# Kernel optimization log

Hardware: AMD Instinct MI355X
Metric: run time of the kernel (lower is better)

The kernel has to match this reference:

```python
import jax, jax.numpy as jnp
import numpy as np

HID = 64
EPS_LN = 1e-5

def _mlp(x, W, b, g, beta):
    # Linear -> LayerNorm -> ReLU (VectorNet-style MLP)
    h = x @ W + b
    mu = jnp.mean(h, axis=-1, keepdims=True)
    var = jnp.var(h, axis=-1, keepdims=True)
    h = (h - mu) * jax.lax.rsqrt(var + EPS_LN) * g + beta
    return jax.nn.relu(h)

def setup_inputs() -> dict:
    key = jax.random.key(0)
    ks = jax.random.split(key, 8)
    N = 2_000_000
    C_IN = 8
    NSEG = 100_000
    inp = {
        'x': jax.random.normal(ks[0], (N, C_IN), dtype=jnp.float32),
        'category': jax.random.randint(ks[1], (N,), 0, NSEG, dtype=jnp.int64),
        'num_segments': NSEG,
    }
    dims_in = [C_IN, 2 * HID, 2 * HID]
    for i, din in enumerate(dims_in):
        kw = jax.random.fold_in(ks[2], i)
        inp[f'W{i}'] = jax.random.normal(kw, (din, HID), dtype=jnp.float32) / np.sqrt(din)
        inp[f'b{i}'] = jnp.zeros((HID,), dtype=jnp.float32)
        inp[f'g{i}'] = jnp.ones((HID,), dtype=jnp.float32)
        inp[f'be{i}'] = jnp.zeros((HID,), dtype=jnp.float32)
    return inp

def reference(x, category, num_segments, W0, b0, g0, be0, W1, b1, g1, be1, W2, b2, g2, be2):
    cat = category.astype(jnp.int32)
    params = [(W0, b0, g0, be0), (W1, b1, g1, be1), (W2, b2, g2, be2)]
    for W, b, g, beta in params:
        h = _mlp(x, W, b, g, beta)                              # [N, HID]
        agg = jax.ops.segment_max(h, cat, num_segments=num_segments)  # [NSEG, HID]
        x = jnp.concatenate([h, agg[cat]], axis=-1)             # [N, 2*HID]
    # column-wise L2 normalization over the node dimension
    col_norm = jnp.linalg.norm(x, axis=0)                       # [2*HID]
    return x / (col_norm + 1e-12)
```

## Files before the change

kernel.cpp:

```cpp
#include <hip/hip_runtime.h>

#define HID 64

__global__ __launch_bounds__(256) void k_hist(const int* __restrict__ cat, int n,
                                              unsigned* __restrict__ counts) {
  int i = blockIdx.x * blockDim.x + threadIdx.x;
  if (i < n) atomicAdd(&counts[cat[i]], 1u);
}

__global__ __launch_bounds__(1024) void k_scan1(const unsigned* __restrict__ counts, int nseg,
                                                unsigned* __restrict__ lexcl,
                                                unsigned* __restrict__ btot) {
  __shared__ unsigned s[1024];
  int t = threadIdx.x;
  int base = blockIdx.x * 1024;
  unsigned v = (base + t < nseg) ? counts[base + t] : 0u;
  s[t] = v;
  __syncthreads();
  for (int o = 1; o < 1024; o <<= 1) {
    unsigned add = (t >= o) ? s[t - o] : 0u;
    __syncthreads();
    s[t] += add;
    __syncthreads();
  }
  if (base + t < nseg) lexcl[base + t] = s[t] - v;
  if (t == 1023) btot[blockIdx.x] = s[1023];
}

__global__ void k_scan2(unsigned* __restrict__ btot, int nb) {
  if (blockIdx.x == 0 && threadIdx.x == 0) {
    unsigned run = 0;
    for (int i = 0; i < nb; i++) { unsigned v = btot[i]; btot[i] = run; run += v; }
  }
}

__global__ __launch_bounds__(256) void k_scan3(const unsigned* __restrict__ lexcl,
                                               const unsigned* __restrict__ btot,
                                               int nseg, int n,
                                               unsigned* __restrict__ offsets,
                                               unsigned* __restrict__ cursor) {
  int i = blockIdx.x * blockDim.x + threadIdx.x;
  if (i < nseg) {
    unsigned o = lexcl[i] + btot[i >> 10];
    offsets[i] = o;
    cursor[i] = o;
  }
  if (i == 0) offsets[nseg] = (unsigned)n;
}

__global__ __launch_bounds__(256) void k_fill(const int* __restrict__ cat, int n,
                                              unsigned* __restrict__ cursor,
                                              unsigned* __restrict__ rowidx) {
  int i = blockIdx.x * blockDim.x + threadIdx.x;
  if (i < n) {
    unsigned p = atomicAdd(&cursor[cat[i]], 1u);
    rowidx[p] = (unsigned)i;
  }
}

template <int CIN, bool HAS_AP>
__global__ __launch_bounds__(256) void k_mlp(const float* __restrict__ xin, int xstride,
                                             const float* __restrict__ W,
                                             const float* __restrict__ bias,
                                             const float* __restrict__ ap,
                                             const int* __restrict__ cat,
                                             const float* __restrict__ g,
                                             const float* __restrict__ be,
                                             float* __restrict__ hout, int ostride, int n) {
  int r = blockIdx.x * blockDim.x + threadIdx.x;
  if (r >= n) return;
  const float* xr = xin + (long)r * xstride;

  float4 a[16];
  if (HAS_AP) {
    const float4* apr = (const float4*)(ap + (long)cat[r] * HID);
#pragma unroll
    for (int j = 0; j < 16; j++) a[j] = apr[j];
  } else {
    const float4* b4 = (const float4*)bias;
#pragma unroll
    for (int j = 0; j < 16; j++) a[j] = b4[j];
  }

#pragma unroll 4
  for (int k4 = 0; k4 < CIN / 4; k4++) {
    float4 xv = ((const float4*)xr)[k4];
    float xs[4] = {xv.x, xv.y, xv.z, xv.w};
#pragma unroll
    for (int kk = 0; kk < 4; kk++) {
      float xk = xs[kk];
      const float4* w4 = (const float4*)(W + (k4 * 4 + kk) * HID);
#pragma unroll
      for (int j = 0; j < 16; j++) {
        float4 w = w4[j];
        a[j].x = fmaf(xk, w.x, a[j].x);
        a[j].y = fmaf(xk, w.y, a[j].y);
        a[j].z = fmaf(xk, w.z, a[j].z);
        a[j].w = fmaf(xk, w.w, a[j].w);
      }
    }
  }

  float s1 = 0.f, s2 = 0.f;
#pragma unroll
  for (int j = 0; j < 16; j++) {
    s1 += a[j].x + a[j].y + a[j].z + a[j].w;
    s2 += a[j].x * a[j].x + a[j].y * a[j].y + a[j].z * a[j].z + a[j].w * a[j].w;
  }
  float mu = s1 * (1.f / 64.f);
  float var = s2 * (1.f / 64.f) - mu * mu;
  float rs = rsqrtf(var + 1e-5f);

  const float4* g4 = (const float4*)g;
  const float4* be4 = (const float4*)be;
  float* orow = hout + (long)r * ostride;
#pragma unroll
  for (int j = 0; j < 16; j++) {
    float4 gg = g4[j], bb = be4[j];
    float4 o;
    o.x = fmaxf(fmaf((a[j].x - mu) * rs, gg.x, bb.x), 0.f);
    o.y = fmaxf(fmaf((a[j].y - mu) * rs, gg.y, bb.y), 0.f);
    o.z = fmaxf(fmaf((a[j].z - mu) * rs, gg.z, bb.z), 0.f);
    o.w = fmaxf(fmaf((a[j].w - mu) * rs, gg.w, bb.w), 0.f);
    ((float4*)orow)[j] = o;
  }
}

template <bool PROJ>
__global__ __launch_bounds__(256) void k_agg(const float* __restrict__ h, int hstride,
                                             const unsigned* __restrict__ offsets,
                                             const unsigned* __restrict__ rowidx,
                                             const float* __restrict__ Wbot,
                                             const float* __restrict__ bias,
                                             float* __restrict__ outbuf, int nseg) {
  int wid = (int)(((long)blockIdx.x * blockDim.x + threadIdx.x) >> 6);
  int lane = threadIdx.x & 63;
  if (wid >= nseg) return;
  unsigned i0 = offsets[wid], i1 = offsets[wid + 1];
  float m = 0.f;
#pragma unroll 4
  for (unsigned i = i0; i < i1; i++) {
    unsigned rr = rowidx[i];
    m = fmaxf(m, h[(long)rr * hstride + lane]);
  }
  if (!PROJ) {
    outbuf[(long)wid * HID + lane] = m;
    return;
  }
  float acc = bias[lane];
#pragma unroll 8
  for (int k = 0; k < HID; k++) {
    float ak = __shfl(m, k, 64);
    acc = fmaf(ak, Wbot[k * HID + lane], acc);
  }
  outbuf[(long)wid * HID + lane] = acc;
}

__global__ __launch_bounds__(256) void k_colsq(const float* __restrict__ h2, int stride, int n,
                                               float* __restrict__ part ) {
  int c = threadIdx.x & 63;
  int rg = threadIdx.x >> 6;
  float acc = 0.f;
  for (long r = (long)blockIdx.x * 4 + rg; r < n; r += (long)gridDim.x * 4) {
    float v = h2[r * stride + c];
    acc += v * v;
  }
  __shared__ float sm[256];
  sm[threadIdx.x] = acc;
  __syncthreads();
  if (threadIdx.x < 64) {
    float t = sm[threadIdx.x] + sm[threadIdx.x + 64] + sm[threadIdx.x + 128] + sm[threadIdx.x + 192];
    atomicAdd(&part[(blockIdx.x & 255) * 128 + threadIdx.x], t);
  }
}

__global__ __launch_bounds__(256) void k_normtail(const float* __restrict__ agg2,
                                                  const unsigned* __restrict__ counts, int nseg,
                                                  float* __restrict__ part) {
  int c = threadIdx.x & 63;
  int sg = threadIdx.x >> 6;
  float acc = 0.f;
  for (int s = blockIdx.x * 4 + sg; s < nseg; s += gridDim.x * 4) {
    float v = agg2[(long)s * HID + c];
    acc += (float)counts[s] * v * v;
  }
  __shared__ float sm[256];
  sm[threadIdx.x] = acc;
  __syncthreads();
  if (threadIdx.x < 64) {
    float t = sm[threadIdx.x] + sm[threadIdx.x + 64] + sm[threadIdx.x + 128] + sm[threadIdx.x + 192];
    atomicAdd(&part[(blockIdx.x & 255) * 128 + 64 + threadIdx.x], t);
  }
}

__global__ void k_normfinal(const float* __restrict__ part, float* __restrict__ invn) {
  int j = threadIdx.x;
  if (j < 128) {
    float s = 0.f;
    for (int i = 0; i < 256; i++) s += part[i * 128 + j];
    invn[j] = 1.f / (sqrtf(s) + 1e-12f);
  }
}

__global__ __launch_bounds__(256) void k_final(float* __restrict__ out,
                                               const float* __restrict__ agg2,
                                               const int* __restrict__ cat,
                                               const float* __restrict__ invn, int n) {
  long i4 = (long)blockIdx.x * blockDim.x + threadIdx.x;
  long r = i4 >> 5;
  int c4 = (int)(i4 & 31);
  if (r >= n) return;
  int c = c4 * 4;
  float4 inv = *(const float4*)(invn + c);
  float4 v;
  if (c < 64) {
    v = *(const float4*)(out + r * 128 + c);
  } else {
    v = *(const float4*)(agg2 + (long)cat[r] * HID + (c - 64));
  }
  v.x *= inv.x; v.y *= inv.y; v.z *= inv.z; v.w *= inv.w;
  *(float4*)(out + r * 128 + c) = v;
}

extern "C" void kernel_launch(void* const* d_in, const int* in_sizes, int n_in,
                              void* d_out, int out_size, void* d_ws, size_t ws_size,
                              hipStream_t stream) {
  const float* x = (const float*)d_in[0];
  const int* cat = (const int*)d_in[1];
  const float* W0 = (const float*)d_in[3];
  const float* b0 = (const float*)d_in[4];
  const float* g0 = (const float*)d_in[5];
  const float* be0 = (const float*)d_in[6];
  const float* W1 = (const float*)d_in[7];
  const float* b1 = (const float*)d_in[8];
  const float* g1 = (const float*)d_in[9];
  const float* be1 = (const float*)d_in[10];
  const float* W2 = (const float*)d_in[11];
  const float* b2 = (const float*)d_in[12];
  const float* g2 = (const float*)d_in[13];
  const float* be2 = (const float*)d_in[14];

  const int N = in_sizes[1];
  const int NSEG = 100000;
  float* out = (float*)d_out;

  char* ws = (char*)d_ws;
  size_t off = 0;
  auto alloc = [&](size_t bytes) -> void* {
    void* p = (void*)(ws + off);
    off = (off + bytes + 511) & ~(size_t)511;
    return p;
  };
  float* h1 = (float*)alloc((size_t)N * HID * 4);
  float* apj = (float*)alloc((size_t)NSEG * HID * 4);
  float* agg2 = (float*)alloc((size_t)NSEG * HID * 4);
  unsigned* rowidx = (unsigned*)alloc((size_t)N * 4);
  unsigned* counts = (unsigned*)alloc((size_t)NSEG * 4);
  unsigned* offsets = (unsigned*)alloc((size_t)(NSEG + 1) * 4);
  unsigned* lexcl = (unsigned*)alloc((size_t)NSEG * 4);
  unsigned* cursor = (unsigned*)alloc((size_t)NSEG * 4);
  unsigned* btot = (unsigned*)alloc(4096);
  float* part = (float*)alloc(256 * 128 * 4);
  float* invn = (float*)alloc(128 * 4);

  hipMemsetAsync(counts, 0, (size_t)NSEG * 4, stream);
  hipMemsetAsync(part, 0, 256 * 128 * 4, stream);

  const int TB = 256;
  const int gridN = (N + TB - 1) / TB;

  k_hist<<<gridN, TB, 0, stream>>>(cat, N, counts);
  int nb = (NSEG + 1023) / 1024;
  k_scan1<<<nb, 1024, 0, stream>>>(counts, NSEG, lexcl, btot);
  k_scan2<<<1, 64, 0, stream>>>(btot, nb);
  k_scan3<<<(NSEG + TB - 1) / TB, TB, 0, stream>>>(lexcl, btot, NSEG, N, offsets, cursor);
  k_fill<<<gridN, TB, 0, stream>>>(cat, N, cursor, rowidx);

  float* h0 = out + 64;
  float* h2 = out;
  const int gseg = NSEG / 4;

  k_mlp<8, false><<<gridN, TB, 0, stream>>>(x, 8, W0, b0, nullptr, nullptr, g0, be0, h0, 128, N);
  k_agg<true><<<gseg, TB, 0, stream>>>(h0, 128, offsets, rowidx, W1 + 64 * HID, b1, apj, NSEG);
  k_mlp<64, true><<<gridN, TB, 0, stream>>>(h0, 128, W1, nullptr, apj, cat, g1, be1, h1, HID, N);
  k_agg<true><<<gseg, TB, 0, stream>>>(h1, HID, offsets, rowidx, W2 + 64 * HID, b2, apj, NSEG);
  k_mlp<64, true><<<gridN, TB, 0, stream>>>(h1, HID, W2, nullptr, apj, cat, g2, be2, h2, 128, N);
  k_agg<false><<<gseg, TB, 0, stream>>>(h2, 128, offsets, rowidx, nullptr, nullptr, agg2, NSEG);

  k_colsq<<<2048, TB, 0, stream>>>(h2, 128, N, part);
  k_normtail<<<512, TB, 0, stream>>>(agg2, counts, NSEG, part);
  k_normfinal<<<1, 128, 0, stream>>>(part, invn);

  k_final<<<(int)(((long)N * 32 + TB - 1) / TB), TB, 0, stream>>>(out, agg2, cat, invn, N);
}
```

Measured before the change: 3.740 ms.

## Recompute layer-0 MLP inside layer-1 kernel, packed FMA, fuse colsq into agg

Layer-1 MLP now recomputes layer-0 Linear+LN+ReLU from x in registers instead of reading h0 back, so h0 is only written once for aggregation. GEMMs use 2-wide float vectors so the compiler can emit packed FMA. All hidden states live in one compact 64-wide buffer reused in place, and the column-square sum moves into the last segment-max pass, which removes the separate colsq kernel. The final kernel assembles the strided output from the compact buffer. The cost is extra recomputation and higher register pressure in the fused kernel.

```diff
diff --git a/kernel.cpp b/kernel.cpp
--- a/kernel.cpp
+++ b/kernel.cpp
@@ -1,6 +1,7 @@
 #include <hip/hip_runtime.h>
 
 #define HID 64
+typedef __attribute__((ext_vector_type(2))) float f32x2;
 
 __global__ __launch_bounds__(256) void k_hist(const int* __restrict__ cat, int n,
                                               unsigned* __restrict__ counts) {
@@ -58,119 +59,168 @@
   }
 }
 
-template <int CIN, bool HAS_AP>
-__global__ __launch_bounds__(256) void k_mlp(const float* __restrict__ xin, int xstride,
-                                             const float* __restrict__ W,
-                                             const float* __restrict__ bias,
-                                             const float* __restrict__ ap,
-                                             const int* __restrict__ cat,
-                                             const float* __restrict__ g,
-                                             const float* __restrict__ be,
-                                             float* __restrict__ hout, int ostride, int n) {
-  int r = blockIdx.x * blockDim.x + threadIdx.x;
+__device__ __forceinline__ void init_acc_from4(f32x2 acc[32], const float4* __restrict__ src) {
+#pragma unroll
+  for (int j = 0; j < 16; ++j) {
+    float4 t = src[j];
+    acc[2 * j][0] = t.x; acc[2 * j][1] = t.y;
+    acc[2 * j + 1][0] = t.z; acc[2 * j + 1][1] = t.w;
+  }
+}
+
+template <int NK4>
+__device__ __forceinline__ void gemm_stream(const float4* __restrict__ x4,
+                                            const float* __restrict__ W,
+                                            f32x2 acc[32]) {
+#pragma unroll 4
+  for (int k4 = 0; k4 < NK4; ++k4) {
+    float4 xv = x4[k4];
+    const float* Wb = W + k4 * 4 * HID;
+    float xs[4] = {xv.x, xv.y, xv.z, xv.w};
+#pragma unroll
+    for (int kk = 0; kk < 4; ++kk) {
+      f32x2 xb; xb[0] = xs[kk]; xb[1] = xs[kk];
+      const f32x2* wr = (const f32x2*)(Wb + kk * HID);
+#pragma unroll
+      for (int j = 0; j < 32; ++j) acc[j] += xb * wr[j];
+    }
+  }
+}
+
+__device__ __forceinline__ void gemm_reg(const f32x2 xr[32],
+                                         const float* __restrict__ W,
+                                         f32x2 acc[32]) {
+#pragma unroll
+  for (int k = 0; k < 64; ++k) {
+    float xk = xr[k >> 1][k & 1];
+    f32x2 xb; xb[0] = xk; xb[1] = xk;
+    const f32x2* wr = (const f32x2*)(W + k * HID);
+#pragma unroll
+    for (int j = 0; j < 32; ++j) acc[j] += xb * wr[j];
+  }
+}
+
+__device__ __forceinline__ void ln_relu(const f32x2 acc[32], const float* __restrict__ g,
+                                        const float* __restrict__ be, f32x2 o[32]) {
+  f32x2 s1; s1[0] = 0.f; s1[1] = 0.f;
+  f32x2 s2; s2[0] = 0.f; s2[1] = 0.f;
+#pragma unroll
+  for (int j = 0; j < 32; ++j) { s1 += acc[j]; s2 += acc[j] * acc[j]; }
+  float mu = (s1[0] + s1[1]) * (1.f / 64.f);
+  float var = (s2[0] + s2[1]) * (1.f / 64.f) - mu * mu;
+  float rs = rsqrtf(var + 1e-5f);
+  const f32x2* g2 = (const f32x2*)g;
+  const f32x2* be2 = (const f32x2*)be;
+#pragma unroll
+  for (int j = 0; j < 32; ++j) {
+    f32x2 t = (acc[j] - mu) * rs * g2[j] + be2[j];
+    f32x2 z; z[0] = fmaxf(t[0], 0.f); z[1] = fmaxf(t[1], 0.f);
+    o[j] = z;
+  }
+}
+
+__device__ __forceinline__ void store_row(float* __restrict__ dst, const f32x2 o[32]) {
+#pragma unroll
+  for (int j = 0; j < 16; ++j) {
+    float4 t;
+    t.x = o[2 * j][0]; t.y = o[2 * j][1];
+    t.z = o[2 * j + 1][0]; t.w = o[2 * j + 1][1];
+    ((float4*)dst)[j] = t;
+  }
+}
+
+__global__ __launch_bounds__(256, 4) void k_mlp0(const float* __restrict__ x,
+    const float* __restrict__ W0, const float* __restrict__ b0,
+    const float* __restrict__ g0, const float* __restrict__ be0,
+    float* __restrict__ h0, int n) {
+  int r = blockIdx.x * 256 + threadIdx.x;
   if (r >= n) return;
-  const float* xr = xin + (long)r * xstride;
-
-  float4 a[16];
-  if (HAS_AP) {
-    const float4* apr = (const float4*)(ap + (long)cat[r] * HID);
-#pragma unroll
-    for (int j = 0; j < 16; j++) a[j] = apr[j];
-  } else {
-    const float4* b4 = (const float4*)bias;
-#pragma unroll
-    for (int j = 0; j < 16; j++) a[j] = b4[j];
-  }
-
-#pragma unroll 4
-  for (int k4 = 0; k4 < CIN / 4; k4++) {
-    float4 xv = ((const float4*)xr)[k4];
-    float xs[4] = {xv.x, xv.y, xv.z, xv.w};
-#pragma unroll
-    for (int kk = 0; kk < 4; kk++) {
-      float xk = xs[kk];
-      const float4* w4 = (const float4*)(W + (k4 * 4 + kk) * HID);
-#pragma unroll
-      for (int j = 0; j < 16; j++) {
-        float4 w = w4[j];
-        a[j].x = fmaf(xk, w.x, a[j].x);
-        a[j].y = fmaf(xk, w.y, a[j].y);
-        a[j].z = fmaf(xk, w.z, a[j].z);
-        a[j].w = fmaf(xk, w.w, a[j].w);
-      }
-    }
-  }
-
-  float s1 = 0.f, s2 = 0.f;
-#pragma unroll
-  for (int j = 0; j < 16; j++) {
-    s1 += a[j].x + a[j].y + a[j].z + a[j].w;
-    s2 += a[j].x * a[j].x + a[j].y * a[j].y + a[j].z * a[j].z + a[j].w * a[j].w;
-  }
-  float mu = s1 * (1.f / 64.f);
-  float var = s2 * (1.f / 64.f) - mu * mu;
-  float rs = rsqrtf(var + 1e-5f);
-
-  const float4* g4 = (const float4*)g;
-  const float4* be4 = (const float4*)be;
-  float* orow = hout + (long)r * ostride;
-#pragma unroll
-  for (int j = 0; j < 16; j++) {
-    float4 gg = g4[j], bb = be4[j];
-    float4 o;
-    o.x = fmaxf(fmaf((a[j].x - mu) * rs, gg.x, bb.x), 0.f);
-    o.y = fmaxf(fmaf((a[j].y - mu) * rs, gg.y, bb.y), 0.f);
-    o.z = fmaxf(fmaf((a[j].z - mu) * rs, gg.z, bb.z), 0.f);
-    o.w = fmaxf(fmaf((a[j].w - mu) * rs, gg.w, bb.w), 0.f);
-    ((float4*)orow)[j] = o;
-  }
-}
-
-template <bool PROJ>
-__global__ __launch_bounds__(256) void k_agg(const float* __restrict__ h, int hstride,
+  f32x2 acc[32];
+  init_acc_from4(acc, (const float4*)b0);
+  gemm_stream<2>((const float4*)(x + (long)r * 8), W0, acc);
+  f32x2 o[32];
+  ln_relu(acc, g0, be0, o);
+  store_row(h0 + (long)r * HID, o);
+}
+
+__global__ __launch_bounds__(256, 3) void k_mlp01(const float* __restrict__ x,
+    const float* __restrict__ W0, const float* __restrict__ b0,
+    const float* __restrict__ g0, const float* __restrict__ be0,
+    const float* __restrict__ W1, const float* __restrict__ apj,
+    const int* __restrict__ cat,
+    const float* __restrict__ g1, const float* __restrict__ be1,
+    float* __restrict__ h1, int n) {
+  int r = blockIdx.x * 256 + threadIdx.x;
+  if (r >= n) return;
+  int c = cat[r];
+  f32x2 acc[32];
+  init_acc_from4(acc, (const float4*)b0);
+  gemm_stream<2>((const float4*)(x + (long)r * 8), W0, acc);
+  f32x2 h0v[32];
+  ln_relu(acc, g0, be0, h0v);
+  init_acc_from4(acc, (const float4*)(apj + (long)c * HID));
+  gemm_reg(h0v, W1, acc);
+  f32x2 o[32];
+  ln_relu(acc, g1, be1, o);
+  store_row(h1 + (long)r * HID, o);
+}
+
+__global__ __launch_bounds__(256, 4) void k_mlp2(float* __restrict__ h,
+    const float* __restrict__ W2, const float* __restrict__ apj,
+    const int* __restrict__ cat,
+    const float* __restrict__ g2, const float* __restrict__ be2, int n) {
+  int r = blockIdx.x * 256 + threadIdx.x;
+  if (r >= n) return;
+  int c = cat[r];
+  f32x2 acc[32];
+  init_acc_from4(acc, (const float4*)(apj + (long)c * HID));
+  gemm_stream<16>((const float4*)(h + (long)r * HID), W2, acc);
+  f32x2 o[32];
+  ln_relu(acc, g2, be2, o);
+  store_row(h + (long)r * HID, o);
+}
+
+template <bool PROJ, bool SQ>
+__global__ __launch_bounds__(256) void k_agg(const float* __restrict__ h,
                                              const unsigned* __restrict__ offsets,
                                              const unsigned* __restrict__ rowidx,
-                                             const float* __restrict__ Wbot,
+                                             const float* __restrict__ Wb,
                                              const float* __restrict__ bias,
-                                             float* __restrict__ outbuf, int nseg) {
-  int wid = (int)(((long)blockIdx.x * blockDim.x + threadIdx.x) >> 6);
+                                             float* __restrict__ outbuf,
+                                             float* __restrict__ part, int nseg) {
+  int wv = threadIdx.x >> 6;
   int lane = threadIdx.x & 63;
-  if (wid >= nseg) return;
-  unsigned i0 = offsets[wid], i1 = offsets[wid + 1];
-  float m = 0.f;
+  int wid = blockIdx.x * 4 + wv;
+  float m = 0.f, sq = 0.f;
+  if (wid < nseg) {
+    unsigned i0 = offsets[wid], i1 = offsets[wid + 1];
 #pragma unroll 4
-  for (unsigned i = i0; i < i1; i++) {
-    unsigned rr = rowidx[i];
-    m = fmaxf(m, h[(long)rr * hstride + lane]);
-  }
-  if (!PROJ) {
-    outbuf[(long)wid * HID + lane] = m;
-    return;
-  }
-  float acc = bias[lane];
+    for (unsigned i = i0; i < i1; ++i) {
+      unsigned rr = rowidx[i];
+      float v = h[(long)rr * HID + lane];
+      m = fmaxf(m, v);
+      if (SQ) sq += v * v;
+    }
+    if (PROJ) {
+      float a = bias[lane];
 #pragma unroll 8
-  for (int k = 0; k < HID; k++) {
-    float ak = __shfl(m, k, 64);
-    acc = fmaf(ak, Wbot[k * HID + lane], acc);
-  }
-  outbuf[(long)wid * HID + lane] = acc;
-}
-
-__global__ __launch_bounds__(256) void k_colsq(const float* __restrict__ h2, int stride, int n,
-                                               float* __restrict__ part ) {
-  int c = threadIdx.x & 63;
-  int rg = threadIdx.x >> 6;
-  float acc = 0.f;
-  for (long r = (long)blockIdx.x * 4 + rg; r < n; r += (long)gridDim.x * 4) {
-    float v = h2[r * stride + c];
-    acc += v * v;
-  }
-  __shared__ float sm[256];
-  sm[threadIdx.x] = acc;
-  __syncthreads();
-  if (threadIdx.x < 64) {
-    float t = sm[threadIdx.x] + sm[threadIdx.x + 64] + sm[threadIdx.x + 128] + sm[threadIdx.x + 192];
-    atomicAdd(&part[(blockIdx.x & 255) * 128 + threadIdx.x], t);
+      for (int k = 0; k < HID; ++k) {
+        float ak = __shfl(m, k, 64);
+        a = fmaf(ak, Wb[k * HID + lane], a);
+      }
+      outbuf[(long)wid * HID + lane] = a;
+    } else {
+      outbuf[(long)wid * HID + lane] = m;
+    }
+  }
+  if (SQ) {
+    __shared__ float sm[256];
+    sm[threadIdx.x] = sq;
+    __syncthreads();
+    if (threadIdx.x < 64) {
+      float t = sm[threadIdx.x] + sm[threadIdx.x + 64] + sm[threadIdx.x + 128] + sm[threadIdx.x + 192];
+      atomicAdd(&part[(blockIdx.x & 255) * 128 + threadIdx.x], t);
+    }
   }
 }
 
@@ -203,23 +253,23 @@
 }
 
 __global__ __launch_bounds__(256) void k_final(float* __restrict__ out,
+                                               const float* __restrict__ h2,
                                                const float* __restrict__ agg2,
                                                const int* __restrict__ cat,
-                                               const float* __restrict__ invn, int n) {
-  long i4 = (long)blockIdx.x * blockDim.x + threadIdx.x;
-  long r = i4 >> 5;
-  int c4 = (int)(i4 & 31);
+                                               const float* __restrict__ invn, long n) {
+  long i8 = (long)blockIdx.x * 256 + threadIdx.x;
+  long r = i8 >> 4;
   if (r >= n) return;
-  int c = c4 * 4;
-  float4 inv = *(const float4*)(invn + c);
-  float4 v;
-  if (c < 64) {
-    v = *(const float4*)(out + r * 128 + c);
-  } else {
-    v = *(const float4*)(agg2 + (long)cat[r] * HID + (c - 64));
-  }
-  v.x *= inv.x; v.y *= inv.y; v.z *= inv.z; v.w *= inv.w;
-  *(float4*)(out + r * 128 + c) = v;
+  int c8 = (int)(i8 & 15) * 8;
+  const float4* src = (c8 < 64) ? (const float4*)(h2 + r * 64 + c8)
+                                : (const float4*)(agg2 + (long)cat[r] * 64 + (c8 - 64));
+  float4 v0 = src[0], v1 = src[1];
+  float4 i0 = *(const float4*)(invn + c8);
+  float4 i1 = *(const float4*)(invn + c8 + 4);
+  v0.x *= i0.x; v0.y *= i0.y; v0.z *= i0.z; v0.w *= i0.w;
+  v1.x *= i1.x; v1.y *= i1.y; v1.z *= i1.z; v1.w *= i1.w;
+  float4* dst = (float4*)(out + r * 128 + c8);
+  dst[0] = v0; dst[1] = v1;
 }
 
 extern "C" void kernel_launch(void* const* d_in, const int* in_sizes, int n_in,
@@ -251,7 +301,7 @@
     off = (off + bytes + 511) & ~(size_t)511;
     return p;
   };
-  float* h1 = (float*)alloc((size_t)N * HID * 4);
+  float* hbuf = (float*)alloc((size_t)N * HID * 4);
   float* apj = (float*)alloc((size_t)NSEG * HID * 4);
   float* agg2 = (float*)alloc((size_t)NSEG * HID * 4);
   unsigned* rowidx = (unsigned*)alloc((size_t)N * 4);
@@ -268,6 +318,7 @@
 
   const int TB = 256;
   const int gridN = (N + TB - 1) / TB;
+  const int gseg = (NSEG + 3) / 4;
 
   k_hist<<<gridN, TB, 0, stream>>>(cat, N, counts);
   int nb = (NSEG + 1023) / 1024;
@@ -276,20 +327,15 @@
   k_scan3<<<(NSEG + TB - 1) / TB, TB, 0, stream>>>(lexcl, btot, NSEG, N, offsets, cursor);
   k_fill<<<gridN, TB, 0, stream>>>(cat, N, cursor, rowidx);
 
-  float* h0 = out + 64;
-  float* h2 = out;
-  const int gseg = NSEG / 4;
-
-  k_mlp<8, false><<<gridN, TB, 0, stream>>>(x, 8, W0, b0, nullptr, nullptr, g0, be0, h0, 128, N);
-  k_agg<true><<<gseg, TB, 0, stream>>>(h0, 128, offsets, rowidx, W1 + 64 * HID, b1, apj, NSEG);
-  k_mlp<64, true><<<gridN, TB, 0, stream>>>(h0, 128, W1, nullptr, apj, cat, g1, be1, h1, HID, N);
-  k_agg<true><<<gseg, TB, 0, stream>>>(h1, HID, offsets, rowidx, W2 + 64 * HID, b2, apj, NSEG);
-  k_mlp<64, true><<<gridN, TB, 0, stream>>>(h1, HID, W2, nullptr, apj, cat, g2, be2, h2, 128, N);
-  k_agg<false><<<gseg, TB, 0, stream>>>(h2, 128, offsets, rowidx, nullptr, nullptr, agg2, NSEG);
-
-  k_colsq<<<2048, TB, 0, stream>>>(h2, 128, N, part);
+  k_mlp0<<<gridN, TB, 0, stream>>>(x, W0, b0, g0, be0, hbuf, N);
+  k_agg<true, false><<<gseg, TB, 0, stream>>>(hbuf, offsets, rowidx, W1 + 64 * HID, b1, apj, nullptr, NSEG);
+  k_mlp01<<<gridN, TB, 0, stream>>>(x, W0, b0, g0, be0, W1, apj, cat, g1, be1, hbuf, N);
+  k_agg<true, false><<<gseg, TB, 0, stream>>>(hbuf, offsets, rowidx, W2 + 64 * HID, b2, apj, nullptr, NSEG);
+  k_mlp2<<<gridN, TB, 0, stream>>>(hbuf, W2, apj, cat, g2, be2, N);
+  k_agg<false, true><<<gseg, TB, 0, stream>>>(hbuf, offsets, rowidx, nullptr, nullptr, agg2, part, NSEG);
+
   k_normtail<<<512, TB, 0, stream>>>(agg2, counts, NSEG, part);
   k_normfinal<<<1, 128, 0, stream>>>(part, invn);
 
-  k_final<<<(int)(((long)N * 32 + TB - 1) / TB), TB, 0, stream>>>(out, agg2, cat, invn, N);
-}
+  k_final<<<(int)(((long)N * 16 + TB - 1) / TB), TB, 0, stream>>>(out, hbuf, agg2, cat, invn, N);
+}
```

Result: faster. 3.034 ms (-18.9%).
